# Optimization experiments

Measured on AMD Instinct MI355X. Metric: run time of the kernel, lower is better.

Reference implementation:

```python
import jax, jax.numpy as jnp
import numpy as np

B, T, V, F = 4, 8, 256, 64

def setup_inputs() -> dict:
    key = jax.random.key(0)
    kx, ka = jax.random.split(key)
    x = jax.random.normal(kx, (B, T, V, F), dtype=jnp.float32)
    # keras 'uniform' initializer: U(-0.05, 0.05), shape (F, 1)
    a = jax.random.uniform(ka, (F, 1), dtype=jnp.float32, minval=-0.05, maxval=0.05)
    return {"x": x, "a": a}

def reference(x, a):
    # x: [B,T,V,F], a: [F,1]
    # diff[b,t,i,j,f] = x[b,t,i,f] - x[b,t,j,f]   (matches tf broadcast+transpose)
    diff = x[:, :, :, None, :] - x[:, :, None, :, :]          # [B,T,V,V,F]
    # project |diff| with learned vector, relu then exp
    scores = jnp.einsum('btijf,f->btij', jnp.abs(diff), a[:, 0])
    tmpS = jnp.exp(jax.nn.relu(scores))                        # [B,T,V,V]
    # original normalizer: S[n,i,j] = tmpS[n,i,j] / sum_k tmpS[n,k,i]
    denom = tmpS.sum(axis=2)                                   # [B,T,V] (sum over i)
    S = tmpS / denom[:, :, :, None]                            # divide by denom[b,t,i]
    return S
```

## Files before the change

### kernel.cpp

```cpp
#include <hip/hip_runtime.h>

constexpr int B = 4, T = 8, V = 256, F = 64;
constexpr int BT = B * T;
constexpr int CHUNK = 4;
constexpr int NCHUNK = V / CHUNK;
constexpr int NXCD = 8;
constexpr int K4 = F / 4;

typedef float v2f __attribute__((ext_vector_type(2)));

__global__ __launch_bounds__(256)
void gl_fused(const float* __restrict__ X, const float* __restrict__ A,
              float* __restrict__ OUT)
{
    const int tid = threadIdx.x;
    const int lb  = (blockIdx.x & (NXCD - 1)) * (BT * NCHUNK / NXCD)
                  + (blockIdx.x >> 3);
    const int bt  = lb >> 6;
    const int ic  = lb & (NCHUNK - 1);
    const int i0  = ic * CHUNK;

    const float* xbt = X + (size_t)bt * V * F;
    const float4* xrow4 = reinterpret_cast<const float4*>(xbt + (size_t)i0 * F);
    const float4* a4    = reinterpret_cast<const float4*>(A);

    __shared__ float wpart[4][CHUNK];
    __shared__ float rden[CHUNK];

    v2f acc2[CHUNK];
#pragma unroll
    for (int r = 0; r < CHUNK; ++r) acc2[r] = (v2f){0.0f, 0.0f};

    const float4* colp = reinterpret_cast<const float4*>(xbt + (size_t)tid * F);
#pragma unroll 4
    for (int k = 0; k < K4; ++k) {
        const float4 xv = colp[k];
        const float4 av = a4[k];
        const v2f xlo = (v2f){xv.x, xv.y};
        const v2f xhi = (v2f){xv.z, xv.w};
        const v2f alo = (v2f){av.x, av.y};
        const v2f ahi = (v2f){av.z, av.w};
#pragma unroll
        for (int r = 0; r < CHUNK; ++r) {
            const float4 sr = xrow4[r * K4 + k];
            const v2f d0 = xlo - (v2f){sr.x, sr.y};
            const v2f d1 = xhi - (v2f){sr.z, sr.w};
            const v2f a0 = __builtin_elementwise_max(d0, -d0);
            const v2f a1 = __builtin_elementwise_max(d1, -d1);
            acc2[r] = __builtin_elementwise_fma(a0, alo, acc2[r]);
            acc2[r] = __builtin_elementwise_fma(a1, ahi, acc2[r]);
        }
    }

    float tmp[CHUNK];
#pragma unroll
    for (int r = 0; r < CHUNK; ++r) {
        const float s = acc2[r].x + acc2[r].y;
        tmp[r] = __expf(fmaxf(s, 0.0f));
    }

    const int lane = tid & 63;
    const int wv   = tid >> 6;
#pragma unroll
    for (int r = 0; r < CHUNK; ++r) {
        float v = tmp[r];
        v += __shfl_xor(v, 32);
        v += __shfl_xor(v, 16);
        v += __shfl_xor(v, 8);
        v += __shfl_xor(v, 4);
        v += __shfl_xor(v, 2);
        v += __shfl_xor(v, 1);
        if (lane == 0) wpart[wv][r] = v;
    }
    __syncthreads();
    if (tid < CHUNK) {
        const float d = wpart[0][tid] + wpart[1][tid] + wpart[2][tid] + wpart[3][tid];
        rden[tid] = 1.0f / d;
    }
    __syncthreads();

    float* obase = OUT + (((size_t)bt * V + i0) * V) + tid;
#pragma unroll
    for (int r = 0; r < CHUNK; ++r)
        obase[(size_t)r * V] = tmp[r] * rden[r];
}

extern "C" void kernel_launch(void* const* d_in, const int* in_sizes, int n_in,
                              void* d_out, int out_size, void* d_ws, size_t ws_size,
                              hipStream_t stream)
{
    const float* X = (const float*)d_in[0];
    const float* A = (const float*)d_in[1];
    float* OUT = (float*)d_out;

    dim3 grid(BT * NCHUNK), block(256);
    gl_fused<<<grid, block, 0, stream>>>(X, A, OUT);
}
```

Measured before the change: 74.26 us.

## Use single-wave blocks with 4-column register tile per thread

Each block now runs as a single 64-thread wavefront, and each thread computes four j columns instead of one. The row operands xrow4 are loaded once and reused across four columns in registers, and the cross-wave shared-memory reduction and both __syncthreads are dropped in favour of wave shuffles alone. In exchange there are four times fewer threads in flight and higher register pressure, which may reduce latency hiding since each column stream is still read directly from global memory.

```diff
diff --git a/kernel.cpp b/kernel.cpp
--- a/kernel.cpp
+++ b/kernel.cpp
@@ -3,17 +3,18 @@
 constexpr int B = 4, T = 8, V = 256, F = 64;
 constexpr int BT = B * T;
 constexpr int CHUNK = 4;
+constexpr int JTILE = 4;
 constexpr int NCHUNK = V / CHUNK;
 constexpr int NXCD = 8;
 constexpr int K4 = F / 4;
 
 typedef float v2f __attribute__((ext_vector_type(2)));
 
-__global__ __launch_bounds__(256)
+__global__ __launch_bounds__(64)
 void gl_fused(const float* __restrict__ X, const float* __restrict__ A,
               float* __restrict__ OUT)
 {
-    const int tid = threadIdx.x;
+    const int t = threadIdx.x;
     const int lb  = (blockIdx.x & (NXCD - 1)) * (BT * NCHUNK / NXCD)
                   + (blockIdx.x >> 3);
     const int bt  = lb >> 6;
@@ -24,65 +25,72 @@
     const float4* xrow4 = reinterpret_cast<const float4*>(xbt + (size_t)i0 * F);
     const float4* a4    = reinterpret_cast<const float4*>(A);
 
-    __shared__ float wpart[4][CHUNK];
-    __shared__ float rden[CHUNK];
+    const float4* cp0 = reinterpret_cast<const float4*>(xbt + (size_t)(t      ) * F);
+    const float4* cp1 = reinterpret_cast<const float4*>(xbt + (size_t)(t +  64) * F);
+    const float4* cp2 = reinterpret_cast<const float4*>(xbt + (size_t)(t + 128) * F);
+    const float4* cp3 = reinterpret_cast<const float4*>(xbt + (size_t)(t + 192) * F);
 
-    v2f acc2[CHUNK];
+    v2f acc[CHUNK][JTILE];
 #pragma unroll
-    for (int r = 0; r < CHUNK; ++r) acc2[r] = (v2f){0.0f, 0.0f};
+    for (int r = 0; r < CHUNK; ++r)
+#pragma unroll
+        for (int jt = 0; jt < JTILE; ++jt) acc[r][jt] = (v2f){0.0f, 0.0f};
 
-    const float4* colp = reinterpret_cast<const float4*>(xbt + (size_t)tid * F);
 #pragma unroll 4
     for (int k = 0; k < K4; ++k) {
-        const float4 xv = colp[k];
-        const float4 av = a4[k];
-        const v2f xlo = (v2f){xv.x, xv.y};
-        const v2f xhi = (v2f){xv.z, xv.w};
+        const float4 xv0 = cp0[k], xv1 = cp1[k], xv2 = cp2[k], xv3 = cp3[k];
+        const float4 av  = a4[k];
         const v2f alo = (v2f){av.x, av.y};
         const v2f ahi = (v2f){av.z, av.w};
+        const v2f xlo[JTILE] = {{xv0.x, xv0.y}, {xv1.x, xv1.y},
+                                {xv2.x, xv2.y}, {xv3.x, xv3.y}};
+        const v2f xhi[JTILE] = {{xv0.z, xv0.w}, {xv1.z, xv1.w},
+                                {xv2.z, xv2.w}, {xv3.z, xv3.w}};
 #pragma unroll
         for (int r = 0; r < CHUNK; ++r) {
             const float4 sr = xrow4[r * K4 + k];
-            const v2f d0 = xlo - (v2f){sr.x, sr.y};
-            const v2f d1 = xhi - (v2f){sr.z, sr.w};
-            const v2f a0 = __builtin_elementwise_max(d0, -d0);
-            const v2f a1 = __builtin_elementwise_max(d1, -d1);
-            acc2[r] = __builtin_elementwise_fma(a0, alo, acc2[r]);
-            acc2[r] = __builtin_elementwise_fma(a1, ahi, acc2[r]);
+            const v2f slo = (v2f){sr.x, sr.y};
+            const v2f shi = (v2f){sr.z, sr.w};
+#pragma unroll
+            for (int jt = 0; jt < JTILE; ++jt) {
+                const v2f d0 = xlo[jt] - slo;
+                const v2f d1 = xhi[jt] - shi;
+                const v2f b0 = __builtin_elementwise_max(d0, -d0);
+                const v2f b1 = __builtin_elementwise_max(d1, -d1);
+                acc[r][jt] = __builtin_elementwise_fma(b0, alo, acc[r][jt]);
+                acc[r][jt] = __builtin_elementwise_fma(b1, ahi, acc[r][jt]);
+            }
         }
     }
 
-    float tmp[CHUNK];
+    float tmp[CHUNK][JTILE];
+#pragma unroll
+    for (int r = 0; r < CHUNK; ++r)
+#pragma unroll
+        for (int jt = 0; jt < JTILE; ++jt) {
+            const float s = acc[r][jt].x + acc[r][jt].y;
+            tmp[r][jt] = __expf(fmaxf(s, 0.0f));
+        }
+
+    float rd[CHUNK];
 #pragma unroll
     for (int r = 0; r < CHUNK; ++r) {
-        const float s = acc2[r].x + acc2[r].y;
-        tmp[r] = __expf(fmaxf(s, 0.0f));
+        float p = (tmp[r][0] + tmp[r][1]) + (tmp[r][2] + tmp[r][3]);
+        p += __shfl_xor(p, 32);
+        p += __shfl_xor(p, 16);
+        p += __shfl_xor(p, 8);
+        p += __shfl_xor(p, 4);
+        p += __shfl_xor(p, 2);
+        p += __shfl_xor(p, 1);
+        rd[r] = 1.0f / p;
     }
 
-    const int lane = tid & 63;
-    const int wv   = tid >> 6;
-#pragma unroll
-    for (int r = 0; r < CHUNK; ++r) {
-        float v = tmp[r];
-        v += __shfl_xor(v, 32);
-        v += __shfl_xor(v, 16);
-        v += __shfl_xor(v, 8);
-        v += __shfl_xor(v, 4);
-        v += __shfl_xor(v, 2);
-        v += __shfl_xor(v, 1);
-        if (lane == 0) wpart[wv][r] = v;
-    }
-    __syncthreads();
-    if (tid < CHUNK) {
-        const float d = wpart[0][tid] + wpart[1][tid] + wpart[2][tid] + wpart[3][tid];
-        rden[tid] = 1.0f / d;
-    }
-    __syncthreads();
-
-    float* obase = OUT + (((size_t)bt * V + i0) * V) + tid;
+    float* ob = OUT + (((size_t)bt * V + i0) * V);
 #pragma unroll
     for (int r = 0; r < CHUNK; ++r)
-        obase[(size_t)r * V] = tmp[r] * rden[r];
+#pragma unroll
+        for (int jt = 0; jt < JTILE; ++jt)
+            ob[(size_t)r * V + jt * 64 + t] = tmp[r][jt] * rd[r];
 }
 
 extern "C" void kernel_launch(void* const* d_in, const int* in_sizes, int n_in,
@@ -93,6 +101,6 @@
     const float* A = (const float*)d_in[1];
     float* OUT = (float*)d_out;
 
-    dim3 grid(BT * NCHUNK), block(256);
+    dim3 grid(BT * NCHUNK), block(64);
     gl_fused<<<grid, block, 0, stream>>>(X, A, OUT);
 }
```

Measured after the change: 74.64 us. No clear change (+0.5%).
